# Kernel tuning notes

Measured on AMD Instinct MI355X. Metric: run time of the kernel, lower is better.

## Reference

```python
import jax, jax.numpy as jnp
import numpy as np

K = 1.0          # curvature of all manifolds
EPS = 1e-6
LN_EPS = 1e-5    # torch LayerNorm eps
POWER_K = 3.0

N_NODES, N_EDGES, IN_DIM, HID, HEADS = 50000, 250000, 128, 32, 4


def _time(s):
    # Lorentz time coordinate from space part
    return jnp.sqrt(jnp.sum(s * s, axis=-1, keepdims=True) + K)


def _hyp_point(s):
    return jnp.concatenate([_time(s), s], axis=-1)


def _layernorm(s, g, b):
    m = jnp.mean(s, axis=-1, keepdims=True)
    v = jnp.var(s, axis=-1, keepdims=True)
    return (s - m) / jnp.sqrt(v + LN_EPS) * g + b


def _fp(x, p=POWER_K):
    # ||x||_2 / ||x^p||_2 * x^p  (TransConv.fp)
    nx = jnp.sqrt(jnp.sum(x * x, axis=-1, keepdims=True))
    xp = x ** p
    nxp = jnp.sqrt(jnp.sum(xp * xp, axis=-1, keepdims=True))
    return nx / nxp * xp


def setup_inputs() -> dict:
    key = jax.random.key(0)
    ks = jax.random.split(key, 12)
    f32 = jnp.float32
    inp = {
        'h': jax.random.normal(ks[0], (N_NODES, IN_DIM), f32),
        'src': jax.random.randint(ks[1], (N_EDGES,), 0, N_NODES, jnp.int32),
        'dst': jax.random.randint(ks[2], (N_EDGES,), 0, N_NODES, jnp.int32),
        # fcs[0][0]: HypLinear(in_dim -> hidden), euclidean input (+1 time col)
        'W_fc': (jax.random.normal(ks[3], (IN_DIM + 1, HID), f32) / np.float32(np.sqrt(IN_DIM + 1))),
        'b_fc': jnp.zeros((HID,), f32),
        # bns[0]: HypLayerNorm(hidden)
        'ln1_g': jnp.ones((HID,), f32), 'ln1_b': jnp.zeros((HID,), f32),
        # Wq/Wk/Wv: per-head HypLinear(hidden -> hidden), input is (hidden+1)-dim point
        'Wq': jax.random.normal(ks[4], (HEADS, HID + 1, HID), f32) / np.float32(np.sqrt(HID + 1)),
        'bq': jnp.zeros((HEADS, HID), f32),
        'Wk': jax.random.normal(ks[5], (HEADS, HID + 1, HID), f32) / np.float32(np.sqrt(HID + 1)),
        'bk': jnp.zeros((HEADS, HID), f32),
        'Wv': jax.random.normal(ks[6], (HEADS, HID + 1, HID), f32) / np.float32(np.sqrt(HID + 1)),
        'bv': jnp.zeros((HEADS, HID), f32),
        # hidden_to_out[0]: HypLinear(hidden -> hidden)
        'W_ho': jax.random.normal(ks[7], (HID + 1, HID), f32) / np.float32(np.sqrt(HID + 1)),
        'b_ho': jnp.zeros((HID,), f32),
        # final HypLayerNorm (self.bn)
        'ln2_g': jnp.ones((HID,), f32), 'ln2_b': jnp.zeros((HID,), f32),
        'norm_scale': jnp.ones((), f32),
    }
    return inp


def reference(h, src, dst, W_fc, b_fc, ln1_g, ln1_b, Wq, bq, Wk, bk, Wv, bv,
              W_ho, b_ho, ln2_g, ln2_b, norm_scale):
    N = h.shape[0]
    # iter == 0: lift euclidean features, prepend ones for time column
    x1 = jnp.concatenate([jnp.ones_like(h[..., :1]), h], axis=-1)  # [N, IN+1]
    hyp = _hyp_point(x1 @ W_fc + b_fc)                             # [N, HID+1]
    residual = hyp
    # HypLayerNorm -> HypActivation(leaky_relu) -> HypDropout (eval: identity).
    # Intermediate time coords are recomputed/discarded; only the final point's
    # full (HID+1) coords feed the q/k/v HypLinears.
    s = jax.nn.leaky_relu(_layernorm(hyp[..., 1:], ln1_g, ln1_b))
    node = _hyp_point(s)                                           # [N, HID+1]
    # per-head HypLinear; edge_attention only uses the space part [:, :, 1:],
    # so the q/k/v time coords are never consumed and are omitted here.
    q = jnp.einsum('nt,htd->nhd', node, Wq) + bq                   # [N, H, HID]
    k = jnp.einsum('nt,htd->nhd', node, Wk) + bk
    v = jnp.einsum('nt,htd->nhd', node, Wv) + bv
    # gather to edges
    qe = q[dst]                                                    # [E, H, HID]
    ke = k[src]
    ve = v[src]
    inv_scale = 1.0 / jnp.abs(norm_scale)
    phi_q = _fp((jax.nn.leaky_relu(qe) + EPS) * inv_scale)
    phi_k = _fp((jax.nn.leaky_relu(ke) + EPS) * inv_scale)
    phi_v = (jax.nn.leaky_relu(ve) + EPS) * inv_scale
    # global (over all edges) kernelized linear attention moments
    ktv = jnp.einsum('ehm,ehd->hmd', phi_k, phi_v)                 # [H, HID, HID]
    numerator = jnp.einsum('ehm,hmd->ehd', phi_q, ktv)             # [E, H, HID]
    denominator = jnp.einsum('ehd,hd->eh', phi_q, jnp.sum(phi_k, axis=0))[..., None]
    attn = jnp.mean(numerator / (denominator + EPS), axis=1)       # [E, HID]
    t = jnp.sqrt(jnp.sum(attn * attn, axis=-1, keepdims=True) + K)
    edge_in = jnp.concatenate([t, attn], axis=-1)                  # [E, HID+1]
    edge_out = _hyp_point(edge_in @ W_ho + b_ho)                   # [E, HID+1]
    # fn.copy_e + fn.mean over incoming edges per destination node
    seg_sum = jax.ops.segment_sum(edge_out, dst, num_segments=N)
    cnt = jax.ops.segment_sum(jnp.ones((edge_out.shape[0], 1), edge_out.dtype), dst, num_segments=N)
    agg = jnp.where(cnt > 0, seg_sum / jnp.maximum(cnt, 1.0), 0.0)
    # Lorentz mid_point of (agg, residual)
    ave = 0.5 * (agg + residual)
    inner = -ave[..., :1] ** 2 + jnp.sum(ave[..., 1:] ** 2, axis=-1, keepdims=True)
    denom = jnp.sqrt(jnp.maximum(jnp.abs(inner), EPS))
    hnew = jnp.sqrt(K) * ave / denom
    # final HypLayerNorm + HypDropout(eval)
    out = _hyp_point(_layernorm(hnew[..., 1:], ln2_g, ln2_b))
    return out
```

## Files before the change

### kernel.cpp

```cpp
#include <hip/hip_runtime.h>

#define NN 50000
#define NE 250000
#define KTVC 4224
#define NBX 512

__device__ __forceinline__ float lrelu(float x) { return x > 0.f ? x : 0.01f * x; }

__global__ __launch_bounds__(256) void k_zero(int* __restrict__ p) {
    int i = blockIdx.x * 256 + threadIdx.x;
    if (i < 100000) p[i] = 0;
}

__global__ __launch_bounds__(256) void k_hist(const int* __restrict__ src,
                                              const int* __restrict__ dst,
                                              int* __restrict__ cnt_src,
                                              int* __restrict__ cnt_dst) {
    int e = blockIdx.x * 256 + threadIdx.x;
    if (e < NE) {
        atomicAdd(&cnt_src[src[e]], 1);
        atomicAdd(&cnt_dst[dst[e]], 1);
    }
}

__global__ __launch_bounds__(512) void k_fc(const float* __restrict__ h,
                                            const float* __restrict__ Wfc,
                                            const float* __restrict__ bfc,
                                            const float* __restrict__ g1,
                                            const float* __restrict__ b1,
                                            float* __restrict__ resid,
                                            float* __restrict__ node33T) {
    __shared__ float hch[128][33];
    __shared__ float stat_t[8][128];
    __shared__ float stat2_t[4][128];
    const int tid = threadIdx.x;
    const int q = __builtin_amdgcn_readfirstlane((threadIdx.x >> 7) & 3);
    const int nl = tid & 127;
    const int base = blockIdx.x * 128;
    const int n = base + nl;

    float acc[8];
#pragma unroll
    for (int jj = 0; jj < 8; ++jj) acc[jj] = Wfc[q * 8 + jj] + bfc[q * 8 + jj];

    for (int c = 0; c < 4; ++c) {
        __syncthreads();
#pragma unroll
        for (int r = 0; r < 8; ++r) {
            int idx = r * 512 + tid;
            int sn = idx >> 5, t = idx & 31;
            int gn = base + sn;
            hch[sn][t] = h[(size_t)((gn < NN) ? gn : 0) * 128 + c * 32 + t];
        }
        __syncthreads();
        for (int i = 0; i < 32; ++i) {
            float hv = hch[nl][i];
            const float* wr = Wfc + (size_t)(1 + c * 32 + i) * 32 + q * 8;
#pragma unroll
            for (int jj = 0; jj < 8; ++jj) acc[jj] = fmaf(hv, wr[jj], acc[jj]);
        }
    }
    float ps = 0.f, pq2 = 0.f;
#pragma unroll
    for (int jj = 0; jj < 8; ++jj) { ps += acc[jj]; pq2 += acc[jj] * acc[jj]; }
    stat_t[q * 2 + 0][nl] = ps;
    stat_t[q * 2 + 1][nl] = pq2;
    __syncthreads();
    float sm = stat_t[0][nl] + stat_t[2][nl] + stat_t[4][nl] + stat_t[6][nl];
    float sq = stat_t[1][nl] + stat_t[3][nl] + stat_t[5][nl] + stat_t[7][nl];
    float mean = sm * (1.f / 32.f);
    float var = fmaxf(sq * (1.f / 32.f) - mean * mean, 0.f);
    float rstd = rsqrtf(var + 1e-5f);
    float lr[8];
    float pl2 = 0.f;
#pragma unroll
    for (int jj = 0; jj < 8; ++jj) {
        int j = q * 8 + jj;
        float ln = (acc[jj] - mean) * rstd * g1[j] + b1[j];
        lr[jj] = lrelu(ln);
        pl2 += lr[jj] * lr[jj];
    }
    stat2_t[q][nl] = pl2;
    __syncthreads();
    float l2 = stat2_t[0][nl] + stat2_t[1][nl] + stat2_t[2][nl] + stat2_t[3][nl];
    if (n < NN) {
        float* rrow = resid + (size_t)n * 36;
#pragma unroll
        for (int jj = 0; jj < 8; ++jj) rrow[1 + q * 8 + jj] = acc[jj];
#pragma unroll
        for (int jj = 0; jj < 8; ++jj) node33T[(size_t)(1 + q * 8 + jj) * NN + n] = lr[jj];
        if (q == 0) {
            rrow[0] = sqrtf(sq + 1.f);
            node33T[n] = sqrtf(l2 + 1.f);
        }
    }
}

__global__ __launch_bounds__(128) void k_qkv(const float* __restrict__ node33T,
                                             const float* __restrict__ Wk, const float* __restrict__ bk,
                                             const float* __restrict__ Wv, const float* __restrict__ bv,
                                             const float* __restrict__ nscale,
                                             const int* __restrict__ cnt_src,
                                             float* __restrict__ partial) {
    __shared__ float nlds[64][33];
    __shared__ float pk[64][36];
    __shared__ float pv[64][36];
    const int tid = threadIdx.x;
    const int w_u = __builtin_amdgcn_readfirstlane(tid >> 6);
    const int h_u = __builtin_amdgcn_readfirstlane(blockIdx.y);
    const int lane = tid & 63;
    const float inv = 1.f / fabsf(nscale[0]);
    const float* W = ((w_u == 0) ? Wk : Wv) + (size_t)h_u * 33 * 32;
    const float* bb = ((w_u == 0) ? bk : bv) + h_u * 32;
    const int mm4 = lane >> 3, d4 = lane & 7;

    float facc[16];
#pragma unroll
    for (int t = 0; t < 16; ++t) facc[t] = 0.f;
    float ks[4] = {0.f, 0.f, 0.f, 0.f};

    const int ntiles = (NN + 63) / 64;
    for (int tile = blockIdx.x; tile < ntiles; tile += NBX) {
        const int base = tile * 64;
        const int n = base + lane;
        for (int idx = tid; idx < 2112; idx += 128) {
            int c = idx >> 6, sn = idx & 63;
            int gn = base + sn;
            nlds[sn][c] = node33T[(size_t)c * NN + ((gn < NN) ? gn : 0)];
        }
        __syncthreads();

        float acc[32];
#pragma unroll
        for (int j = 0; j < 32; ++j) acc[j] = bb[j];
        for (int i = 0; i < 33; ++i) {
            float hv = nlds[lane][i];
            const float* wr = W + (size_t)i * 32;
#pragma unroll
            for (int j = 0; j < 32; ++j) acc[j] = fmaf(hv, wr[j], acc[j]);
        }

        if (w_u == 0) {
            const float wc = (n < NN) ? (float)cnt_src[n] : 0.f;
            float s2 = 0.f, s6 = 0.f;
#pragma unroll
            for (int j = 0; j < 32; ++j) {
                float x = (lrelu(acc[j]) + 1e-6f) * inv;
                s2 += x * x;
                float x3 = x * x * x;
                s6 += x3 * x3;
                acc[j] = x3;
            }
            const float factor = sqrtf(s2) / sqrtf(s6) * wc;
#pragma unroll
            for (int j = 0; j < 32; ++j) pk[lane][j] = factor * acc[j];
        } else {
#pragma unroll
            for (int j = 0; j < 32; ++j) pv[lane][j] = (lrelu(acc[j]) + 1e-6f) * inv;
        }
        __syncthreads();

#pragma unroll 4
        for (int n0 = 0; n0 < 32; ++n0) {
            const int nn = w_u * 32 + n0;
            float4 pkv = *(const float4*)&pk[nn][mm4 * 4];
            float4 pvv = *(const float4*)&pv[nn][d4 * 4];
            float pkv_a[4] = {pkv.x, pkv.y, pkv.z, pkv.w};
            float pvv_a[4] = {pvv.x, pvv.y, pvv.z, pvv.w};
#pragma unroll
            for (int i = 0; i < 4; ++i)
#pragma unroll
                for (int jj = 0; jj < 4; ++jj)
                    facc[i * 4 + jj] = fmaf(pkv_a[i], pvv_a[jj], facc[i * 4 + jj]);
            if (d4 == 0) {
#pragma unroll
                for (int i = 0; i < 4; ++i) ks[i] += pkv_a[i];
            }
        }
        __syncthreads();
    }

    float* scr = &pk[0][0];
    float* scr2 = &pv[0][0];
    if (w_u == 0) {
#pragma unroll
        for (int t = 0; t < 16; ++t) scr[lane * 16 + t] = facc[t];
        if (d4 == 0) {
#pragma unroll
            for (int i = 0; i < 4; ++i) scr2[mm4 * 4 + i] = ks[i];
        }
    }
    __syncthreads();
    if (w_u == 1) {
        float* pb = partial + (size_t)blockIdx.x * KTVC + h_u * 1056;
#pragma unroll
        for (int i = 0; i < 4; ++i)
#pragma unroll
            for (int jj = 0; jj < 4; ++jj)
                pb[(mm4 * 4 + i) * 32 + d4 * 4 + jj] =
                    facc[i * 4 + jj] + scr[lane * 16 + i * 4 + jj];
        if (d4 == 0) {
#pragma unroll
            for (int i = 0; i < 4; ++i)
                pb[1024 + mm4 * 4 + i] = ks[i] + scr2[mm4 * 4 + i];
        }
    }
}

__global__ __launch_bounds__(256) void k_red(const float* __restrict__ partial,
                                             float* __restrict__ ktvf) {
    __shared__ float red[8][33];
    const int tid = threadIdx.x;
    const int col = tid & 31, g = tid >> 5;
    const int c = blockIdx.x * 32 + col;
    float s = 0.f;
    for (int r = g * 64; r < (g + 1) * 64; ++r)
        s += partial[(size_t)r * KTVC + c];
    red[g][col] = s;
    __syncthreads();
    if (tid < 32) {
        float t0 = (red[0][tid] + red[1][tid]) + (red[2][tid] + red[3][tid]);
        float t1 = (red[4][tid] + red[5][tid]) + (red[6][tid] + red[7][tid]);
        ktvf[blockIdx.x * 32 + tid] = t0 + t1;
    }
}

__global__ __launch_bounds__(256) void k_final(const float* __restrict__ node33T,
                                               const float* __restrict__ Wq, const float* __restrict__ bq,
                                               const float* __restrict__ nscale,
                                               const float* __restrict__ ktvf,
                                               const float* __restrict__ Who,
                                               const float* __restrict__ bho,
                                               const float* __restrict__ g2,
                                               const float* __restrict__ b2,
                                               const int* __restrict__ cnt_dst,
                                               const float* __restrict__ resid,
                                               float* __restrict__ out) {
    __shared__ float nlds[64][37];
    __shared__ float att[4][64][33];
    __shared__ float who_lds[33 * 32];
    __shared__ float g2l[32], b2l[32], bhol[32];
    const int tid = threadIdx.x;
    const int h_u = __builtin_amdgcn_readfirstlane(tid >> 6);
    const int lane = tid & 63;
    const int base = blockIdx.x * 64;
    const float inv = 1.f / fabsf(nscale[0]);

#pragma unroll
    for (int r = 0; r < 9; ++r) {
        int idx = r * 256 + tid;
        if (idx < 2112) {
            int c = idx >> 6, sn = idx & 63;
            int gn = base + sn;
            nlds[sn][c] = node33T[(size_t)c * NN + ((gn < NN) ? gn : 0)];
        }
    }
    for (int f = tid; f < 33 * 32; f += 256) who_lds[f] = Who[f];
    if (tid < 32) { g2l[tid] = g2[tid]; b2l[tid] = b2[tid]; bhol[tid] = bho[tid]; }
    __syncthreads();

    {
        float acc[32];
#pragma unroll
        for (int j = 0; j < 32; ++j) acc[j] = bq[h_u * 32 + j];
        const float* W = Wq + (size_t)h_u * 33 * 32;
        for (int i = 0; i < 33; ++i) {
            float hv = nlds[lane][i];
            const float* wr = W + (size_t)i * 32;
#pragma unroll
            for (int j = 0; j < 32; ++j) acc[j] = fmaf(hv, wr[j], acc[j]);
        }
        float s2 = 0.f, s6 = 0.f;
#pragma unroll
        for (int j = 0; j < 32; ++j) {
            float x = (lrelu(acc[j]) + 1e-6f) * inv;
            s2 += x * x;
            float x3 = x * x * x;
            s6 += x3 * x3;
            acc[j] = x3;
        }
        const float factor = sqrtf(s2) / sqrtf(s6);
        const float* ksum = ktvf + h_u * 1056 + 1024;
        float den = 0.f;
#pragma unroll
        for (int j = 0; j < 32; ++j) { acc[j] *= factor; den += acc[j] * ksum[j]; }
        const float rd = 0.25f / (den + 1e-6f);
        float num[32];
#pragma unroll
        for (int d = 0; d < 32; ++d) num[d] = 0.f;
        const float* kt = ktvf + h_u * 1056;
#pragma unroll 2
        for (int t = 0; t < 32; ++t) {
            const float f = acc[t];
            const float* kr = kt + t * 32;
#pragma unroll
            for (int d = 0; d < 32; ++d) num[d] = fmaf(f, kr[d], num[d]);
        }
#pragma unroll
        for (int d = 0; d < 32; ++d) att[h_u][lane][d] = num[d] * rd;
    }
    __syncthreads();

    const int nl2 = tid >> 2, jq = tid & 3;
    const int n2 = base + nl2;
    const int nc = (n2 < NN) ? n2 : NN - 1;
    float attn[32];
#pragma unroll
    for (int d = 0; d < 32; ++d)
        attn[d] = ((att[0][nl2][d] + att[1][nl2][d]) + (att[2][nl2][d] + att[3][nl2][d]));
    float a2 = 0.f;
#pragma unroll
    for (int d = 0; d < 32; ++d) a2 += attn[d] * attn[d];
    const float tc = sqrtf(a2 + 1.f);
    float eo[8];
#pragma unroll
    for (int jj = 0; jj < 8; ++jj) {
        int j = jq * 8 + jj;
        eo[jj] = bhol[j] + tc * who_lds[j];
    }
#pragma unroll
    for (int d = 0; d < 32; ++d) {
        const float f = attn[d];
        const float* wr = &who_lds[(1 + d) * 32 + jq * 8];
#pragma unroll
        for (int jj = 0; jj < 8; ++jj) eo[jj] = fmaf(f, wr[jj], eo[jj]);
    }
    float e2 = 0.f;
#pragma unroll
    for (int jj = 0; jj < 8; ++jj) e2 += eo[jj] * eo[jj];
    e2 += __shfl_xor(e2, 1);
    e2 += __shfl_xor(e2, 2);
    const float te = sqrtf(e2 + 1.f);
    const float sc = (cnt_dst[nc] > 0) ? 1.f : 0.f;
    const float* rr = resid + (size_t)nc * 36;
    const float av0 = 0.5f * (sc * te + rr[0]);
    float avs[8];
    float pinner = 0.f;
#pragma unroll
    for (int jj = 0; jj < 8; ++jj) {
        avs[jj] = 0.5f * (sc * eo[jj] + rr[1 + jq * 8 + jj]);
        pinner += avs[jj] * avs[jj];
    }
    pinner += __shfl_xor(pinner, 1);
    pinner += __shfl_xor(pinner, 2);
    const float inner = pinner - av0 * av0;
    const float rdn = 1.f / sqrtf(fmaxf(fabsf(inner), 1e-6f));
    float pm = 0.f;
#pragma unroll
    for (int jj = 0; jj < 8; ++jj) { avs[jj] *= rdn; pm += avs[jj]; }
    pm += __shfl_xor(pm, 1);
    pm += __shfl_xor(pm, 2);
    const float mean = pm * (1.f / 32.f);
    float pv2 = 0.f;
#pragma unroll
    for (int jj = 0; jj < 8; ++jj) { float dd = avs[jj] - mean; pv2 += dd * dd; }
    pv2 += __shfl_xor(pv2, 1);
    pv2 += __shfl_xor(pv2, 2);
    const float rstd = rsqrtf(pv2 * (1.f / 32.f) + 1e-5f);
    float ln[8];
    float pl2 = 0.f;
#pragma unroll
    for (int jj = 0; jj < 8; ++jj) {
        int j = jq * 8 + jj;
        ln[jj] = (avs[jj] - mean) * rstd * g2l[j] + b2l[j];
        pl2 += ln[jj] * ln[jj];
    }
    pl2 += __shfl_xor(pl2, 1);
    pl2 += __shfl_xor(pl2, 2);
    if (n2 < NN) {
        float* orow = out + (size_t)n2 * 33;
#pragma unroll
        for (int jj = 0; jj < 8; ++jj) orow[1 + jq * 8 + jj] = ln[jj];
        if (jq == 0) orow[0] = sqrtf(pl2 + 1.f);
    }
}

extern "C" void kernel_launch(void* const* d_in, const int* in_sizes, int n_in,
                              void* d_out, int out_size, void* d_ws, size_t ws_size,
                              hipStream_t stream) {
    const float* h   = (const float*)d_in[0];
    const int* src   = (const int*)d_in[1];
    const int* dst   = (const int*)d_in[2];
    const float* Wfc = (const float*)d_in[3];
    const float* bfc = (const float*)d_in[4];
    const float* g1  = (const float*)d_in[5];
    const float* b1  = (const float*)d_in[6];
    const float* Wq  = (const float*)d_in[7];
    const float* bq  = (const float*)d_in[8];
    const float* Wk  = (const float*)d_in[9];
    const float* bk  = (const float*)d_in[10];
    const float* Wv  = (const float*)d_in[11];
    const float* bv  = (const float*)d_in[12];
    const float* Who = (const float*)d_in[13];
    const float* bho = (const float*)d_in[14];
    const float* g2  = (const float*)d_in[15];
    const float* b2  = (const float*)d_in[16];
    const float* nsc = (const float*)d_in[17];
    float* out = (float*)d_out;
    char* ws = (char*)d_ws;

    int* cnt_src   = (int*)(ws + 0);
    int* cnt_dst   = (int*)(ws + 200000);
    float* resid   = (float*)(ws + 400000);
    float* node33T = (float*)(ws + 7600000);
    float* part    = (float*)(ws + 14200000);
    float* ktvf    = (float*)(ws + 22852608);

    hipLaunchKernelGGL(k_zero, dim3(391), dim3(256), 0, stream, (int*)ws);
    hipLaunchKernelGGL(k_hist, dim3((NE + 255) / 256), dim3(256), 0, stream,
                       src, dst, cnt_src, cnt_dst);
    hipLaunchKernelGGL(k_fc, dim3((NN + 127) / 128), dim3(512), 0, stream,
                       h, Wfc, bfc, g1, b1, resid, node33T);
    hipLaunchKernelGGL(k_qkv, dim3(NBX, 4), dim3(128), 0, stream,
                       node33T, Wk, bk, Wv, bv, nsc, cnt_src, part);
    hipLaunchKernelGGL(k_red, dim3(KTVC / 32), dim3(256), 0, stream,
                       part, ktvf);
    hipLaunchKernelGGL(k_final, dim3((NN + 63) / 64), dim3(256), 0, stream,
                       node33T, Wq, bq, nsc, ktvf, Who, bho, g2, b2, cnt_dst, resid, out);
}
```

Measured before the change: 127.6 us.

## Retune KTV partial grid, unroll GEMM loops, stage KTV in LDS for final kernel

Shrinks the KTV-accumulation grid so each block handles exactly two 64-node tiles with a fully unrolled loop, and adjusts the partial reduction to match the new row count. Unrolls the inner matmul loops in the first linear and the K/V projection. In the final kernel, node features are loaded straight into registers instead of going through LDS, and the per-head KTV matrix and k-sum are staged into LDS and read as float4 vectors instead of scalar global loads. This trades more registers and a larger LDS footprint, which may lower occupancy, for fewer global loads and less loop overhead.

```diff
diff --git a/kernel.cpp b/kernel.cpp
--- a/kernel.cpp
+++ b/kernel.cpp
@@ -3,7 +3,7 @@
 #define NN 50000
 #define NE 250000
 #define KTVC 4224
-#define NBX 512
+#define NBX 391
 
 __device__ __forceinline__ float lrelu(float x) { return x > 0.f ? x : 0.01f * x; }
 
@@ -53,6 +53,7 @@
             hch[sn][t] = h[(size_t)((gn < NN) ? gn : 0) * 128 + c * 32 + t];
         }
         __syncthreads();
+#pragma unroll
         for (int i = 0; i < 32; ++i) {
             float hv = hch[nl][i];
             const float* wr = Wfc + (size_t)(1 + c * 32 + i) * 32 + q * 8;
@@ -119,8 +120,9 @@
     for (int t = 0; t < 16; ++t) facc[t] = 0.f;
     float ks[4] = {0.f, 0.f, 0.f, 0.f};
 
-    const int ntiles = (NN + 63) / 64;
-    for (int tile = blockIdx.x; tile < ntiles; tile += NBX) {
+#pragma unroll
+    for (int half = 0; half < 2; ++half) {
+        const int tile = blockIdx.x + half * NBX;
         const int base = tile * 64;
         const int n = base + lane;
         for (int idx = tid; idx < 2112; idx += 128) {
@@ -133,6 +135,7 @@
         float acc[32];
 #pragma unroll
         for (int j = 0; j < 32; ++j) acc[j] = bb[j];
+#pragma unroll
         for (int i = 0; i < 33; ++i) {
             float hv = nlds[lane][i];
             const float* wr = W + (size_t)i * 32;
@@ -213,8 +216,9 @@
     const int tid = threadIdx.x;
     const int col = tid & 31, g = tid >> 5;
     const int c = blockIdx.x * 32 + col;
+    const int r0 = g * 49, r1 = min(r0 + 49, NBX);
     float s = 0.f;
-    for (int r = g * 64; r < (g + 1) * 64; ++r)
+    for (int r = r0; r < r1; ++r)
         s += partial[(size_t)r * KTVC + c];
     red[g][col] = s;
     __syncthreads();
@@ -236,8 +240,8 @@
                                                const int* __restrict__ cnt_dst,
                                                const float* __restrict__ resid,
                                                float* __restrict__ out) {
-    __shared__ float nlds[64][37];
     __shared__ float att[4][64][33];
+    __shared__ float ktv_l[4][1056];
     __shared__ float who_lds[33 * 32];
     __shared__ float g2l[32], b2l[32], bhol[32];
     const int tid = threadIdx.x;
@@ -245,30 +249,28 @@
     const int lane = tid & 63;
     const int base = blockIdx.x * 64;
     const float inv = 1.f / fabsf(nscale[0]);
-
-#pragma unroll
-    for (int r = 0; r < 9; ++r) {
-        int idx = r * 256 + tid;
-        if (idx < 2112) {
-            int c = idx >> 6, sn = idx & 63;
-            int gn = base + sn;
-            nlds[sn][c] = node33T[(size_t)c * NN + ((gn < NN) ? gn : 0)];
-        }
-    }
+    const int n = base + lane;
+    const int ncl = (n < NN) ? n : 0;
+
+    for (int f = tid; f < KTVC; f += 256) ((float*)ktv_l)[f] = ktvf[f];
     for (int f = tid; f < 33 * 32; f += 256) who_lds[f] = Who[f];
     if (tid < 32) { g2l[tid] = g2[tid]; b2l[tid] = b2[tid]; bhol[tid] = bho[tid]; }
+
+    float nvec[33];
+#pragma unroll
+    for (int c = 0; c < 33; ++c) nvec[c] = node33T[(size_t)c * NN + ncl];
+    float acc[32];
+#pragma unroll
+    for (int j = 0; j < 32; ++j) acc[j] = bq[h_u * 32 + j];
     __syncthreads();
 
     {
-        float acc[32];
-#pragma unroll
-        for (int j = 0; j < 32; ++j) acc[j] = bq[h_u * 32 + j];
         const float* W = Wq + (size_t)h_u * 33 * 32;
+#pragma unroll
         for (int i = 0; i < 33; ++i) {
-            float hv = nlds[lane][i];
             const float* wr = W + (size_t)i * 32;
 #pragma unroll
-            for (int j = 0; j < 32; ++j) acc[j] = fmaf(hv, wr[j], acc[j]);
+            for (int j = 0; j < 32; ++j) acc[j] = fmaf(nvec[i], wr[j], acc[j]);
         }
         float s2 = 0.f, s6 = 0.f;
 #pragma unroll
@@ -280,7 +282,7 @@
             acc[j] = x3;
         }
         const float factor = sqrtf(s2) / sqrtf(s6);
-        const float* ksum = ktvf + h_u * 1056 + 1024;
+        const float* ksum = &ktv_l[h_u][1024];
         float den = 0.f;
 #pragma unroll
         for (int j = 0; j < 32; ++j) { acc[j] *= factor; den += acc[j] * ksum[j]; }
@@ -288,13 +290,18 @@
         float num[32];
 #pragma unroll
         for (int d = 0; d < 32; ++d) num[d] = 0.f;
-        const float* kt = ktvf + h_u * 1056;
-#pragma unroll 2
+#pragma unroll
         for (int t = 0; t < 32; ++t) {
             const float f = acc[t];
-            const float* kr = kt + t * 32;
-#pragma unroll
-            for (int d = 0; d < 32; ++d) num[d] = fmaf(f, kr[d], num[d]);
+            const float* kr = &ktv_l[h_u][t * 32];
+#pragma unroll
+            for (int d4 = 0; d4 < 8; ++d4) {
+                float4 kv = *(const float4*)&kr[d4 * 4];
+                num[d4 * 4 + 0] = fmaf(f, kv.x, num[d4 * 4 + 0]);
+                num[d4 * 4 + 1] = fmaf(f, kv.y, num[d4 * 4 + 1]);
+                num[d4 * 4 + 2] = fmaf(f, kv.z, num[d4 * 4 + 2]);
+                num[d4 * 4 + 3] = fmaf(f, kv.w, num[d4 * 4 + 3]);
+            }
         }
 #pragma unroll
         for (int d = 0; d < 32; ++d) att[h_u][lane][d] = num[d] * rd;
```

Measured after the change: 145.1 us. 1.14x slower.
